# Kernel tuning notes

Measured on AMD Instinct MI355X. Metric: run time of the kernel, lower is better.

Reference implementation:

```python
import jax, jax.numpy as jnp
import numpy as np
from jax import lax

V, E, T, F, K = 100000, 300, 50, 100, 3
B, S = 32, 512


def setup_inputs() -> dict:
    key = jax.random.key(0)
    ks = jax.random.split(key, 10)
    inp = {
        "x": jax.random.randint(ks[0], (B, S), 0, V),
        "tags": jax.random.randint(ks[1], (B, S), 0, T),
        "emb": jax.random.normal(ks[2], (V, E), dtype=jnp.float32),
        "conv_w": jax.random.normal(ks[3], (F, E, K), dtype=jnp.float32) / np.sqrt(E * K),
        "conv_b": jnp.zeros((F,), dtype=jnp.float32),
        "fc_w": jax.random.normal(ks[4], (T, F), dtype=jnp.float32) / np.sqrt(F),
        "fc_b": jnp.zeros((T,), dtype=jnp.float32),
        "start_trans": jax.random.uniform(ks[5], (T,), dtype=jnp.float32, minval=-0.1, maxval=0.1),
        "end_trans": jax.random.uniform(ks[6], (T,), dtype=jnp.float32, minval=-0.1, maxval=0.1),
        "trans": jax.random.uniform(ks[7], (T, T), dtype=jnp.float32, minval=-0.1, maxval=0.1),
    }
    return inp


def _emissions(x, emb, conv_w, conv_b, fc_w, fc_b):
    e = emb[x]                                   # [B,S,E] embedding gather
    e = jnp.transpose(e, (0, 2, 1))              # [B,E,S]
    h = lax.conv_general_dilated(e, conv_w, (1,), [(K // 2, K // 2)])  # [B,F,S] (NCW/OIW)
    h = jax.nn.relu(h + conv_b[None, :, None])   # dropout is identity in eval
    feat = jnp.transpose(h, (0, 2, 1))           # [B,S,F]
    return (jnp.einsum("bsf,tf->bst", feat, fc_w) + fc_b).astype(jnp.float32)  # [B,S,T]


def _crf_nll(emissions, tags, start_trans, end_trans, trans):
    # numerator: score of the gold tag path (full mask)
    em_tag = jnp.take_along_axis(emissions, tags[..., None], axis=-1)[..., 0]  # [B,S]
    num = (start_trans[tags[:, 0]]
           + em_tag.sum(-1)
           + trans[tags[:, :-1], tags[:, 1:]].sum(-1)
           + end_trans[tags[:, -1]])                                           # [B]

    # denominator: forward algorithm via scan over time
    alpha0 = start_trans[None, :] + emissions[:, 0]                             # [B,T]

    def step(alpha, em_t):
        # alpha: [B,T] prev scores; em_t: [B,T] emissions at t
        new = jax.nn.logsumexp(alpha[:, :, None] + trans[None] + em_t[:, None, :], axis=1)
        return new, None

    alpha, _ = lax.scan(step, alpha0, jnp.transpose(emissions[:, 1:], (1, 0, 2)))
    log_z = jax.nn.logsumexp(alpha + end_trans[None, :], axis=-1)               # [B]
    return -(num - log_z).sum()  # torchcrf default reduction='sum'; model returns -llh


def reference(x, tags, emb, conv_w, conv_b, fc_w, fc_b, start_trans, end_trans, trans):
    emissions = _emissions(x, emb, conv_w, conv_b, fc_w, fc_b)
    return _crf_nll(emissions, tags, start_trans, end_trans, trans)
```

## Files before the change

kernel.cpp:

```cpp
#include <hip/hip_runtime.h>
#include <hip/hip_bf16.h>
#include <math.h>

#define BB 32
#define SS 512
#define EE 300
#define FF 100
#define TT 50
#define CH 16
#define NC 32

typedef __attribute__((ext_vector_type(8))) short v8s;
typedef __attribute__((ext_vector_type(4))) float v4f;
#define MFMA16 __builtin_amdgcn_mfma_f32_16x16x32_bf16

#define AP 328
#define NCH 10
#define CKS 3
#define CHB (128 * 96)
#define A2P 136
#define MP 72

__device__ inline unsigned short f2bf(float v) {
    unsigned u = __float_as_uint(v);
    unsigned r = u + 0x7fff + ((u >> 16) & 1);
    return (unsigned short)(r >> 16);
}
__device__ inline float bf2f(short s) {
    return __uint_as_float(((unsigned)(unsigned short)s) << 16);
}
__device__ inline unsigned pkbf2(float a, float b) {
    __hip_bfloat162 h = __float22bfloat162_rn(make_float2(a, b));
    return *(unsigned*)&h;
}
__device__ inline v8s ldsld8(const short* p) {
    return *(const v8s*)__builtin_assume_aligned(p, 16);
}
__device__ inline void g2lds16(const void* g, void* l) {
    __builtin_amdgcn_global_load_lds(
        (const __attribute__((address_space(1))) unsigned int*)g,
        (__attribute__((address_space(3))) unsigned int*)l, 16, 0, 0);
}

__global__ void prep_kernel(const float* __restrict__ tr, const float* __restrict__ cw,
                            const float* __restrict__ fcw,
                            unsigned short* __restrict__ wB2,
                            unsigned short* __restrict__ fcwT2,
                            unsigned short* __restrict__ AT,
                            unsigned short* __restrict__ Ab,
                            float* __restrict__ accum, unsigned* __restrict__ cnt)
{
    const int gid = blockIdx.x * 256 + threadIdx.x;
    const int gs  = 64 * 256;
    if (gid == 0) { *accum = 0.f; *cnt = 0u; }
    for (int idx = gid; idx < NCH * CKS * 8 * 512; idx += gs) {
        int e = idx & 7, p = (idx >> 3) & 63, blk = idx >> 9;
        int ch = blk / 24, rem = blk - ch * 24;
        int sl = rem >> 3, ft = rem & 7;
        int col = p >> 2, q = p & 3;
        int n  = ft * 16 + col;
        int gk = ch * 96 + sl * 32 + q * 8 + e;
        int kk = gk / 320, ee = gk - kk * 320;
        float v = (n < FF && ee < EE) ? cw[n * 900 + ee * 3 + kk] : 0.f;
        wB2[idx] = f2bf(v);
    }
    for (int idx = gid; idx < 16 * 512; idx += gs) {
        int e = idx & 7, p = (idx >> 3) & 63, blk = idx >> 9;
        int ks = blk >> 2, nt = blk & 3;
        int col = p >> 2, q = p & 3;
        int t = nt * 16 + col, f = ks * 32 + q * 8 + e;
        float v = (t < TT && f < FF) ? fcw[t * FF + f] : 0.f;
        fcwT2[idx] = f2bf(v);
    }
    for (int idx = gid; idx < 64 * 64; idx += gs) {
        int r = idx >> 6, c2 = idx & 63;
        AT[idx] = (r < TT && c2 < TT) ? f2bf(__expf(tr[c2 * TT + r])) : 0;
        Ab[idx] = (r < TT && c2 < TT) ? f2bf(__expf(tr[r * TT + c2])) : 0;
    }
}

__global__ __launch_bounds__(256, 3) void emis_kernel(
    const int* __restrict__ x, const float* __restrict__ emb,
    const unsigned short* __restrict__ wB2, const float* __restrict__ cb,
    const unsigned short* __restrict__ fcwT2, const float* __restrict__ fcb,
    const int* __restrict__ tags,
    float* __restrict__ expem, float* __restrict__ rmv, float* __restrict__ emtag)
{
    __shared__ __align__(16) short ldsA[34 * AP];
    __shared__ __align__(16) short ldsB[CHB];

    const int b    = blockIdx.y;
    const int s0   = blockIdx.x * 32;
    const int tid  = threadIdx.x;
    const int wv   = tid >> 6;
    const int lane = tid & 63;
    const int col  = lane & 15;
    const int q    = lane >> 4;
    const int bofs = ((col << 2) | q) << 3;

#pragma unroll
    for (int it = 0; it < 6; ++it) {
        int seg = it * 4 + wv;
        g2lds16((const char*)wB2 + seg * 1024 + lane * 16,
                (char*)ldsB + seg * 1024);
    }

    int   xr[10], ofs[10], e0a[10];
#pragma unroll
    for (int it = 0; it < 10; ++it) {
        int g = tid + it * 256;
        int r = g / 75, eg = g - r * 75;
        int e0 = eg * 4;
        int src = s0 - 1 + r;
        bool v = (g < 2550) && (src >= 0) && (src < SS);
        xr[it]  = v ? x[b * SS + src] : -1;
        ofs[it] = r * AP + e0;
        e0a[it] = e0;
    }
    float4 vv[10];
#pragma unroll
    for (int it = 0; it < 10; ++it)
        vv[it] = (xr[it] >= 0)
               ? *(const float4*)(emb + (size_t)xr[it] * EE + e0a[it])
               : make_float4(0.f, 0.f, 0.f, 0.f);
#pragma unroll
    for (int it = 0; it < 10; ++it) {
        int g = tid + it * 256;
        if (g < 2550) {
            unsigned lo = pkbf2(vv[it].x, vv[it].y);
            unsigned hi = pkbf2(vv[it].z, vv[it].w);
            *(uint2*)&ldsA[ofs[it]] = make_uint2(lo, hi);
        }
    }
    if (tid < 34 * 5) {
        int r = tid / 5, c0 = 300 + (tid % 5) * 4;
        *(short4*)&ldsA[r * AP + c0] = make_short4(0, 0, 0, 0);
    }

    v4f acc[2][2];
#pragma unroll
    for (int a = 0; a < 2; ++a)
#pragma unroll
        for (int f = 0; f < 2; ++f) acc[a][f] = (v4f){0.f, 0.f, 0.f, 0.f};

    const int ftA = wv * 2, ftB = wv * 2 + 1;
    for (int ch = 0; ch < NCH; ++ch) {
        __syncthreads();
#pragma unroll
        for (int sl = 0; sl < CKS; ++sl) {
            int gk = ch * 96 + sl * 32;
            int kk = (gk >= 640) ? 2 : (gk >= 320 ? 1 : 0);
            int e0 = gk - kk * 320;
            v8s a0 = ldsld8(&ldsA[(col + kk) * AP + e0 + q * 8]);
            v8s a1 = ldsld8(&ldsA[(16 + col + kk) * AP + e0 + q * 8]);
            v8s b0 = ldsld8(&ldsB[((sl * 8 + ftA) << 9) + bofs]);
            v8s b1 = ldsld8(&ldsB[((sl * 8 + ftB) << 9) + bofs]);
            acc[0][0] = MFMA16(a0, b0, acc[0][0], 0, 0, 0);
            acc[0][1] = MFMA16(a0, b1, acc[0][1], 0, 0, 0);
            acc[1][0] = MFMA16(a1, b0, acc[1][0], 0, 0, 0);
            acc[1][1] = MFMA16(a1, b1, acc[1][1], 0, 0, 0);
        }
        __syncthreads();
        if (ch < NCH - 1) {
            const char* g = (const char*)(wB2 + (size_t)(ch + 1) * CHB);
#pragma unroll
            for (int it = 0; it < 6; ++it) {
                int seg = it * 4 + wv;
                g2lds16(g + seg * 1024 + lane * 16, (char*)ldsB + seg * 1024);
            }
        }
    }

    short* A2 = ldsA;
    short* B2 = ldsB;
#pragma unroll
    for (int it = 0; it < 4; ++it) {
        int seg = it * 4 + wv;
        g2lds16((const char*)fcwT2 + seg * 1024 + lane * 16,
                (char*)B2 + seg * 1024);
    }
#pragma unroll
    for (int st = 0; st < 2; ++st)
#pragma unroll
        for (int fi = 0; fi < 2; ++fi) {
            int f = (wv * 2 + fi) * 16 + col;
            float bias = (f < FF) ? cb[f] : 0.f;
#pragma unroll
            for (int rg = 0; rg < 4; ++rg) {
                int s = st * 16 + q * 4 + rg;
                float v = (f < FF) ? fmaxf(acc[st][fi][rg] + bias, 0.f) : 0.f;
                A2[s * A2P + f] = (short)f2bf(v);
            }
        }
    __syncthreads();

    if (wv < 2) {
        v4f a2[4];
#pragma unroll
        for (int nt = 0; nt < 4; ++nt) a2[nt] = (v4f){0.f, 0.f, 0.f, 0.f};
#pragma unroll
        for (int ks = 0; ks < 4; ++ks) {
            v8s af = ldsld8(&A2[(wv * 16 + col) * A2P + ks * 32 + q * 8]);
#pragma unroll
            for (int nt = 0; nt < 4; ++nt) {
                v8s bt = ldsld8(&B2[((ks * 4 + nt) << 9) + bofs]);
                a2[nt] = MFMA16(af, bt, a2[nt], 0, 0, 0);
            }
        }
        float fb0 = fcb[col], fb1 = fcb[16 + col], fb2 = fcb[32 + col];
        float fb3 = (col < 2) ? fcb[48 + col] : 0.f;
#pragma unroll
        for (int rg = 0; rg < 4; ++rg) {
            int s = s0 + wv * 16 + q * 4 + rg;
            float e0v = a2[0][rg] + fb0;
            float e1v = a2[1][rg] + fb1;
            float e2v = a2[2][rg] + fb2;
            float e3v = (col < 2) ? a2[3][rg] + fb3 : -1e30f;
            float m = fmaxf(fmaxf(e0v, e1v), fmaxf(e2v, e3v));
#pragma unroll
            for (int off = 1; off < 16; off <<= 1) m = fmaxf(m, __shfl_xor(m, off));
            int gidx = b * SS + s;
            if (col == 0) rmv[gidx] = m;
            int tg = tags[gidx];
            float* orow = expem + (size_t)gidx * TT;
            orow[col]      = __expf(e0v - m);
            orow[16 + col] = __expf(e1v - m);
            orow[32 + col] = __expf(e2v - m);
            if (col < 2) orow[48 + col] = __expf(e3v - m);
            if (tg == col)            emtag[gidx] = e0v;
            else if (tg == 16 + col)  emtag[gidx] = e1v;
            else if (tg == 32 + col)  emtag[gidx] = e2v;
            else if (col < 2 && tg == 48 + col) emtag[gidx] = e3v;
        }
    }
}

__global__ __launch_bounds__(64) void chunk_kernel(
    const float* __restrict__ expem, const unsigned short* __restrict__ AT,
    const unsigned short* __restrict__ Ab,
    unsigned short* __restrict__ R, float* __restrict__ lsR)
{
    __shared__ __align__(16) short L[2][64 * MP];
    __shared__ __align__(16) float emL[CH][64];
    const int c = blockIdx.x, b = blockIdx.y;
    const int lane = threadIdx.x;
    const int col = lane & 15, q = lane >> 4;
    const int t0 = c * CH + 1;
    const int nf = (c == NC - 1) ? (SS - 1 - (NC - 1) * CH) : CH;

    for (int idx = lane; idx < CH * 64; idx += 64) {
        int k = idx >> 6, m = idx & 63;
        float v = 0.f;
        if (m < TT && k < nf) v = expem[((size_t)(b * SS + t0 + k)) * TT + m];
        emL[k][m] = v;
    }

    v8s af[4][2];
#pragma unroll
    for (int jt = 0; jt < 4; ++jt)
#pragma unroll
        for (int kc = 0; kc < 2; ++kc)
            af[jt][kc] = *(const v8s*)(AT + (jt * 16 + col) * 64 + kc * 32 + q * 8);
    __syncthreads();

    {
        const v8s* arow = (const v8s*)(Ab + lane * 64);
#pragma unroll
        for (int g = 0; g < 8; ++g) {
            v8s a = arow[g];
            float f[8];
#pragma unroll
            for (int e = 0; e < 8; ++e) f[e] = bf2f(a[e]) * emL[0][g * 8 + e];
            uint4 o = make_uint4(pkbf2(f[0], f[1]), pkbf2(f[2], f[3]),
                                 pkbf2(f[4], f[5]), pkbf2(f[6], f[7]));
            *(uint4*)&L[0][lane * MP + g * 8] = o;
        }
    }

    int cur = 0;
    for (int k = 1; k < nf; ++k) {
        __syncthreads();
        v8s bf[4][2];
#pragma unroll
        for (int nt = 0; nt < 4; ++nt)
#pragma unroll
            for (int kc = 0; kc < 2; ++kc)
                bf[nt][kc] = ldsld8(&L[cur][(nt * 16 + col) * MP + kc * 32 + q * 8]);
        v4f acc[4][4];
#pragma unroll
        for (int jt = 0; jt < 4; ++jt)
#pragma unroll
            for (int nt = 0; nt < 4; ++nt) {
                acc[jt][nt] = (v4f){0.f, 0.f, 0.f, 0.f};
                acc[jt][nt] = MFMA16(af[jt][0], bf[nt][0], acc[jt][nt], 0, 0, 0);
                acc[jt][nt] = MFMA16(af[jt][1], bf[nt][1], acc[jt][nt], 0, 0, 0);
            }
        if (k < nf - 1) {
#pragma unroll
            for (int jt = 0; jt < 4; ++jt) {
                const float4 em4 = *(const float4*)&emL[k][jt * 16 + q * 4];
#pragma unroll
                for (int nt = 0; nt < 4; ++nt) {
                    uint2 o = make_uint2(
                        pkbf2(acc[jt][nt][0] * em4.x, acc[jt][nt][1] * em4.y),
                        pkbf2(acc[jt][nt][2] * em4.z, acc[jt][nt][3] * em4.w));
                    *(uint2*)&L[cur ^ 1][(nt * 16 + col) * MP + jt * 16 + q * 4] = o;
                }
            }
            cur ^= 1;
        } else {
            float vals[4][4][4];
            float mx = 0.f;
#pragma unroll
            for (int jt = 0; jt < 4; ++jt) {
                const float4 em4 = *(const float4*)&emL[k][jt * 16 + q * 4];
#pragma unroll
                for (int nt = 0; nt < 4; ++nt) {
                    vals[jt][nt][0] = acc[jt][nt][0] * em4.x;
                    vals[jt][nt][1] = acc[jt][nt][1] * em4.y;
                    vals[jt][nt][2] = acc[jt][nt][2] * em4.z;
                    vals[jt][nt][3] = acc[jt][nt][3] * em4.w;
#pragma unroll
                    for (int r = 0; r < 4; ++r) mx = fmaxf(mx, vals[jt][nt][r]);
                }
            }
#pragma unroll
            for (int off = 1; off < 64; off <<= 1) mx = fmaxf(mx, __shfl_xor(mx, off));
            mx = fmaxf(mx, 1e-37f);
            float inv = 1.f / mx;
            unsigned short* Rc = R + ((size_t)(b * NC + c) << 12);
#pragma unroll
            for (int jt = 0; jt < 4; ++jt)
#pragma unroll
                for (int nt = 0; nt < 4; ++nt)
#pragma unroll
                    for (int r = 0; r < 4; ++r)
                        Rc[(jt * 16 + q * 4 + r) * 64 + nt * 16 + col] =
                            f2bf(vals[jt][nt][r] * inv);
            if (lane == 0) lsR[b * NC + c] = __logf(mx);
        }
    }
}

__global__ __launch_bounds__(256) void chain_kernel(
    const float* __restrict__ expem, const unsigned short* __restrict__ R,
    const float* __restrict__ lsR, const float* __restrict__ start,
    const float* __restrict__ endt,
    const float* __restrict__ emtag, const float* __restrict__ rmv,
    const int* __restrict__ tags, const float* __restrict__ tr,
    float* __restrict__ accum, unsigned* __restrict__ cnt,
    float* __restrict__ out)
{
    __shared__ __align__(16) float pvec[64];
    __shared__ float red[8];
    __shared__ float lzsh;
    const int b = blockIdx.x, tid = threadIdx.x;
    const int wv = tid >> 6, i = tid & 63;

    if (wv == 0) {
        pvec[i] = (i < TT) ? __expf(start[i]) * expem[((size_t)(b * SS)) * TT + i] : 0.f;
        const unsigned short* Rb = R + ((size_t)(b * NC) << 12);
        v8s rb[3][8];
#pragma unroll
        for (int pc = 0; pc < 3; ++pc)
#pragma unroll
            for (int g = 0; g < 8; ++g)
                rb[pc][g] = *(const v8s*)(Rb + ((size_t)pc << 12) + i * 64 + g * 8);
        float logacc = 0.f;
#pragma unroll
        for (int c = 0; c < NC; ++c) {
            const int slot = c % 3;
            float acc = 0.f;
            const float4* pv = (const float4*)pvec;
#pragma unroll
            for (int g = 0; g < 8; ++g) {
                v8s v = rb[slot][g];
                float4 pA = pv[g * 2], pB = pv[g * 2 + 1];
                acc = fmaf(bf2f(v[0]), pA.x, acc);
                acc = fmaf(bf2f(v[1]), pA.y, acc);
                acc = fmaf(bf2f(v[2]), pA.z, acc);
                acc = fmaf(bf2f(v[3]), pA.w, acc);
                acc = fmaf(bf2f(v[4]), pB.x, acc);
                acc = fmaf(bf2f(v[5]), pB.y, acc);
                acc = fmaf(bf2f(v[6]), pB.z, acc);
                acc = fmaf(bf2f(v[7]), pB.w, acc);
            }
            if (c + 3 < NC) {
                const unsigned short* Rn = Rb + ((size_t)(c + 3) << 12);
#pragma unroll
                for (int g = 0; g < 8; ++g)
                    rb[slot][g] = *(const v8s*)(Rn + i * 64 + g * 8);
            }
            float mx = acc;
#pragma unroll
            for (int off = 1; off < 64; off <<= 1) mx = fmaxf(mx, __shfl_xor(mx, off));
            mx = fmaxf(mx, 1e-37f);
            logacc += __logf(mx) + lsR[b * NC + c];
            pvec[i] = acc * (1.f / mx);
        }
        float sv = (i < TT) ? pvec[i] * __expf(endt[i]) : 0.f;
#pragma unroll
        for (int off = 1; off < 64; off <<= 1) sv += __shfl_xor(sv, off);
        if (i == 0) lzsh = logacc + __logf(sv);
    } else {
        float accN = 0.f, accR = 0.f;
        for (int s = tid - 64; s < SS; s += 192) {
            int gi = b * SS + s;
            accN += emtag[gi];
            accR += rmv[gi];
            int tg = tags[gi];
            if (s < SS - 1) accN += tr[tg * TT + tags[gi + 1]];
        }
#pragma unroll
        for (int off = 1; off < 64; off <<= 1) {
            accN += __shfl_xor(accN, off);
            accR += __shfl_xor(accR, off);
        }
        if (i == 0) { red[wv] = accN; red[4 + wv] = accR; }
    }
    __syncthreads();
    if (tid == 0) {
        float tn  = red[1] + red[2] + red[3];
        float trm = red[5] + red[6] + red[7];
        float num = tn + start[tags[b * SS]] + endt[tags[b * SS + SS - 1]];
        float nll = trm + lzsh - num;
        atomicAdd(accum, nll);
        __threadfence();
        unsigned old = atomicAdd(cnt, 1u);
        if (old == BB - 1) out[0] = atomicAdd(accum, 0.f);
    }
}

extern "C" void kernel_launch(void* const* d_in, const int* in_sizes, int n_in,
                              void* d_out, int out_size, void* d_ws, size_t ws_size,
                              hipStream_t stream)
{
    const int*   x    = (const int*)d_in[0];
    const int*   tags = (const int*)d_in[1];
    const float* emb  = (const float*)d_in[2];
    const float* cw   = (const float*)d_in[3];
    const float* cb   = (const float*)d_in[4];
    const float* fcw  = (const float*)d_in[5];
    const float* fcb  = (const float*)d_in[6];
    const float* st   = (const float*)d_in[7];
    const float* en   = (const float*)d_in[8];
    const float* tr   = (const float*)d_in[9];

    unsigned short* wB2   = (unsigned short*)d_ws;
    unsigned short* fcwT2 = wB2 + NCH * CKS * 8 * 512;
    unsigned short* ATm   = fcwT2 + 16 * 512;
    unsigned short* Abm   = ATm + 4096;
    unsigned short* Rm    = Abm + 4096;
    float* fbase   = (float*)(Rm + (size_t)BB * NC * 4096);
    float* expem   = fbase;
    float* rmv     = expem + (size_t)BB * SS * TT;
    float* emtag   = rmv + BB * SS;
    float* lsR     = emtag + BB * SS;
    float* accum   = lsR + BB * NC;
    unsigned* cnt  = (unsigned*)(accum + 1);

    prep_kernel<<<dim3(64), 256, 0, stream>>>(tr, cw, fcw, wB2, fcwT2, ATm, Abm,
                                              accum, cnt);
    emis_kernel<<<dim3(16, BB), 256, 0, stream>>>(x, emb, wB2, cb, fcwT2, fcb,
                                                  tags, expem, rmv, emtag);
    chunk_kernel<<<dim3(NC, BB), 64, 0, stream>>>(expem, ATm, Abm, Rm, lsR);
    chain_kernel<<<dim3(BB), 256, 0, stream>>>(expem, Rm, lsR, st, en,
                                               emtag, rmv, tags, tr,
                                               accum, cnt, (float*)d_out);
}
```

Baseline: 241.1 us.

## Fold prep into emissions kernel and chain into chunk kernel via flags

Result: slower. 527.7 us (+118.9%).

```diff
diff --git a/kernel.cpp b/kernel.cpp
--- a/kernel.cpp
+++ b/kernel.cpp
@@ -20,6 +20,7 @@
 #define CHB (128 * 96)
 #define A2P 136
 #define MP 72
+#define MAGICU 0x13572468u
 
 __device__ inline unsigned short f2bf(float v) {
     unsigned u = __float_as_uint(v);
@@ -42,67 +43,68 @@
         (__attribute__((address_space(3))) unsigned int*)l, 16, 0, 0);
 }
 
-__global__ void prep_kernel(const float* __restrict__ tr, const float* __restrict__ cw,
-                            const float* __restrict__ fcw,
-                            unsigned short* __restrict__ wB2,
-                            unsigned short* __restrict__ fcwT2,
-                            unsigned short* __restrict__ AT,
-                            unsigned short* __restrict__ Ab,
-                            float* __restrict__ accum, unsigned* __restrict__ cnt)
-{
-    const int gid = blockIdx.x * 256 + threadIdx.x;
-    const int gs  = 64 * 256;
-    if (gid == 0) { *accum = 0.f; *cnt = 0u; }
-    for (int idx = gid; idx < NCH * CKS * 8 * 512; idx += gs) {
-        int e = idx & 7, p = (idx >> 3) & 63, blk = idx >> 9;
-        int ch = blk / 24, rem = blk - ch * 24;
-        int sl = rem >> 3, ft = rem & 7;
-        int col = p >> 2, q = p & 3;
-        int n  = ft * 16 + col;
-        int gk = ch * 96 + sl * 32 + q * 8 + e;
-        int kk = gk / 320, ee = gk - kk * 320;
-        float v = (n < FF && ee < EE) ? cw[n * 900 + ee * 3 + kk] : 0.f;
-        wB2[idx] = f2bf(v);
-    }
-    for (int idx = gid; idx < 16 * 512; idx += gs) {
-        int e = idx & 7, p = (idx >> 3) & 63, blk = idx >> 9;
-        int ks = blk >> 2, nt = blk & 3;
-        int col = p >> 2, q = p & 3;
-        int t = nt * 16 + col, f = ks * 32 + q * 8 + e;
-        float v = (t < TT && f < FF) ? fcw[t * FF + f] : 0.f;
-        fcwT2[idx] = f2bf(v);
-    }
-    for (int idx = gid; idx < 64 * 64; idx += gs) {
-        int r = idx >> 6, c2 = idx & 63;
-        AT[idx] = (r < TT && c2 < TT) ? f2bf(__expf(tr[c2 * TT + r])) : 0;
-        Ab[idx] = (r < TT && c2 < TT) ? f2bf(__expf(tr[r * TT + c2])) : 0;
-    }
-}
-
 __global__ __launch_bounds__(256, 3) void emis_kernel(
     const int* __restrict__ x, const float* __restrict__ emb,
-    const unsigned short* __restrict__ wB2, const float* __restrict__ cb,
-    const unsigned short* __restrict__ fcwT2, const float* __restrict__ fcb,
-    const int* __restrict__ tags,
+    const float* __restrict__ cw, const float* __restrict__ cb,
+    const float* __restrict__ fcw, const float* __restrict__ fcb,
+    const float* __restrict__ tr, const int* __restrict__ tags,
+    unsigned short* __restrict__ wB2, unsigned short* __restrict__ fcwT2,
+    unsigned short* __restrict__ AT, unsigned short* __restrict__ Ab,
+    unsigned* __restrict__ flags, unsigned* __restrict__ done,
+    float* __restrict__ accum, unsigned* __restrict__ cnt,
     float* __restrict__ expem, float* __restrict__ rmv, float* __restrict__ emtag)
 {
     __shared__ __align__(16) short ldsA[34 * AP];
     __shared__ __align__(16) short ldsB[CHB];
 
-    const int b    = blockIdx.y;
-    const int s0   = blockIdx.x * 32;
-    const int tid  = threadIdx.x;
-    const int wv   = tid >> 6;
-    const int lane = tid & 63;
-    const int col  = lane & 15;
-    const int q    = lane >> 4;
-    const int bofs = ((col << 2) | q) << 3;
-
-#pragma unroll
-    for (int it = 0; it < 6; ++it) {
-        int seg = it * 4 + wv;
-        g2lds16((const char*)wB2 + seg * 1024 + lane * 16,
-                (char*)ldsB + seg * 1024);
+    const int b      = blockIdx.y;
+    const int s0     = blockIdx.x * 32;
+    const int tid    = threadIdx.x;
+    const int wv     = tid >> 6;
+    const int lane   = tid & 63;
+    const int col    = lane & 15;
+    const int q      = lane >> 4;
+    const int bofs   = ((col << 2) | q) << 3;
+    const int linear = blockIdx.y * 16 + blockIdx.x;
+
+    if (linear < 64) {
+        const int gid = linear * 256 + tid;
+        const int gs  = 64 * 256;
+        for (int idx = gid; idx < NCH * CKS * 8 * 512; idx += gs) {
+            int e = idx & 7, p = (idx >> 3) & 63, blk = idx >> 9;
+            int ch = blk / 24, rem = blk - ch * 24;
+            int sl = rem >> 3, ft = rem & 7;
+            int pc = p >> 2, pq = p & 3;
+            int n  = ft * 16 + pc;
+            int gk = ch * 96 + sl * 32 + pq * 8 + e;
+            int kk = gk / 320, ee = gk - kk * 320;
+            float v = (n < FF && ee < EE) ? cw[n * 900 + ee * 3 + kk] : 0.f;
+            wB2[idx] = f2bf(v);
+        }
+        for (int idx = gid; idx < 16 * 512; idx += gs) {
+            int e = idx & 7, p = (idx >> 3) & 63, blk = idx >> 9;
+            int ks = blk >> 2, nt = blk & 3;
+            int pc = p >> 2, pq = p & 3;
+            int t = nt * 16 + pc, f = ks * 32 + pq * 8 + e;
+            float v = (t < TT && f < FF) ? fcw[t * FF + f] : 0.f;
+            fcwT2[idx] = f2bf(v);
+        }
+        for (int idx = gid; idx < 64 * 64; idx += gs) {
+            int r = idx >> 6, c2 = idx & 63;
+            AT[idx] = (r < TT && c2 < TT) ? f2bf(__expf(tr[c2 * TT + r])) : 0;
+            Ab[idx] = (r < TT && c2 < TT) ? f2bf(__expf(tr[r * TT + c2])) : 0;
+        }
+        __syncthreads();
+        if (tid == 0) {
+            __threadfence();
+            __hip_atomic_store(&flags[linear], MAGICU,
+                               __ATOMIC_RELEASE, __HIP_MEMORY_SCOPE_AGENT);
+        }
+    }
+    if (linear == 0) {
+        if (tid < BB) done[tid] = 0u;
+        else if (tid == BB) *accum = 0.f;
+        else if (tid == BB + 1) *cnt = 0u;
     }
 
     int   xr[10], ofs[10], e0a[10];
@@ -135,6 +137,19 @@
     if (tid < 34 * 5) {
         int r = tid / 5, c0 = 300 + (tid % 5) * 4;
         *(short4*)&ldsA[r * AP + c0] = make_short4(0, 0, 0, 0);
+    }
+
+    if (tid == 0) {
+        for (int i = 0; i < 64; ++i)
+            while (__hip_atomic_load(&flags[i], __ATOMIC_ACQUIRE,
+                                     __HIP_MEMORY_SCOPE_AGENT) != MAGICU) {}
+    }
+    __syncthreads();
+#pragma unroll
+    for (int it = 0; it < 6; ++it) {
+        int seg = it * 4 + wv;
+        g2lds16((const char*)wB2 + seg * 1024 + lane * 16,
+                (char*)ldsB + seg * 1024);
     }
 
     v4f acc[2][2];
@@ -238,7 +253,13 @@
 __global__ __launch_bounds__(64) void chunk_kernel(
     const float* __restrict__ expem, const unsigned short* __restrict__ AT,
     const unsigned short* __restrict__ Ab,
-    unsigned short* __restrict__ R, float* __restrict__ lsR)
+    const float* __restrict__ emtag, const float* __restrict__ rmv,
+    const int* __restrict__ tags, const float* __restrict__ tr,
+    const float* __restrict__ start, const float* __restrict__ endt,
+    unsigned short* __restrict__ R, float* __restrict__ lsR,
+    float* __restrict__ part, unsigned* __restrict__ done,
+    float* __restrict__ accum, unsigned* __restrict__ cnt,
+    float* __restrict__ out)
 {
     __shared__ __align__(16) short L[2][64 * MP];
     __shared__ __align__(16) float emL[CH][64];
@@ -248,6 +269,19 @@
     const int t0 = c * CH + 1;
     const int nf = (c == NC - 1) ? (SS - 1 - (NC - 1) * CH) : CH;
 
+    {
+        int s = c * CH + lane;
+        float pc = 0.f;
+        if (lane < CH) {
+            int gi = b * SS + s;
+            pc = rmv[gi] - emtag[gi];
+            if (s < SS - 1) pc -= tr[tags[gi] * TT + tags[gi + 1]];
+        }
+#pragma unroll
+        for (int off = 1; off < 16; off <<= 1) pc += __shfl_xor(pc, off);
+        if (lane == 0) part[b * NC + c] = pc;
+    }
+
     for (int idx = lane; idx < CH * 64; idx += 64) {
         int k = idx >> 6, m = idx & 63;
         float v = 0.f;
@@ -340,94 +374,72 @@
             if (lane == 0) lsR[b * NC + c] = __logf(mx);
         }
     }
-}
-
-__global__ __launch_bounds__(256) void chain_kernel(
-    const float* __restrict__ expem, const unsigned short* __restrict__ R,
-    const float* __restrict__ lsR, const float* __restrict__ start,
-    const float* __restrict__ endt,
-    const float* __restrict__ emtag, const float* __restrict__ rmv,
-    const int* __restrict__ tags, const float* __restrict__ tr,
-    float* __restrict__ accum, unsigned* __restrict__ cnt,
-    float* __restrict__ out)
-{
-    __shared__ __align__(16) float pvec[64];
-    __shared__ float red[8];
-    __shared__ float lzsh;
-    const int b = blockIdx.x, tid = threadIdx.x;
-    const int wv = tid >> 6, i = tid & 63;
-
-    if (wv == 0) {
-        pvec[i] = (i < TT) ? __expf(start[i]) * expem[((size_t)(b * SS)) * TT + i] : 0.f;
-        const unsigned short* Rb = R + ((size_t)(b * NC) << 12);
-        v8s rb[3][8];
-#pragma unroll
-        for (int pc = 0; pc < 3; ++pc)
+
+    int old = 0;
+    if (lane == 0) {
+        __threadfence();
+        old = (int)atomicAdd(&done[b], 1u);
+    }
+    old = __shfl(old, 0);
+    if (old != NC - 1) return;
+    __threadfence();
+
+    float* pvec = (float*)emL;
+    pvec[lane] = (lane < TT) ? __expf(start[lane]) * expem[((size_t)(b * SS)) * TT + lane] : 0.f;
+    const unsigned short* Rb = R + ((size_t)(b * NC) << 12);
+    v8s rb[3][8];
+#pragma unroll
+    for (int pc = 0; pc < 3; ++pc)
+#pragma unroll
+        for (int g = 0; g < 8; ++g)
+            rb[pc][g] = *(const v8s*)(Rb + ((size_t)pc << 12) + lane * 64 + g * 8);
+    float logacc = 0.f;
+#pragma unroll
+    for (int cc = 0; cc < NC; ++cc) {
+        const int slot = cc % 3;
+        float acc = 0.f;
+        const float4* pv = (const float4*)pvec;
+#pragma unroll
+        for (int g = 0; g < 8; ++g) {
+            v8s v = rb[slot][g];
+            float4 pA = pv[g * 2], pB = pv[g * 2 + 1];
+            acc = fmaf(bf2f(v[0]), pA.x, acc);
+            acc = fmaf(bf2f(v[1]), pA.y, acc);
+            acc = fmaf(bf2f(v[2]), pA.z, acc);
+            acc = fmaf(bf2f(v[3]), pA.w, acc);
+            acc = fmaf(bf2f(v[4]), pB.x, acc);
+            acc = fmaf(bf2f(v[5]), pB.y, acc);
+            acc = fmaf(bf2f(v[6]), pB.z, acc);
+            acc = fmaf(bf2f(v[7]), pB.w, acc);
+        }
+        if (cc + 3 < NC) {
+            const unsigned short* Rn = Rb + ((size_t)(cc + 3) << 12);
 #pragma unroll
             for (int g = 0; g < 8; ++g)
-                rb[pc][g] = *(const v8s*)(Rb + ((size_t)pc << 12) + i * 64 + g * 8);
-        float logacc = 0.f;
-#pragma unroll
-        for (int c = 0; c < NC; ++c) {
-            const int slot = c % 3;
-            float acc = 0.f;
-            const float4* pv = (const float4*)pvec;
-#pragma unroll
-            for (int g = 0; g < 8; ++g) {
-                v8s v = rb[slot][g];
-                float4 pA = pv[g * 2], pB = pv[g * 2 + 1];
-                acc = fmaf(bf2f(v[0]), pA.x, acc);
-                acc = fmaf(bf2f(v[1]), pA.y, acc);
-                acc = fmaf(bf2f(v[2]), pA.z, acc);
-                acc = fmaf(bf2f(v[3]), pA.w, acc);
-                acc = fmaf(bf2f(v[4]), pB.x, acc);
-                acc = fmaf(bf2f(v[5]), pB.y, acc);
-                acc = fmaf(bf2f(v[6]), pB.z, acc);
-                acc = fmaf(bf2f(v[7]), pB.w, acc);
-            }
-            if (c + 3 < NC) {
-                const unsigned short* Rn = Rb + ((size_t)(c + 3) << 12);
-#pragma unroll
-                for (int g = 0; g < 8; ++g)
-                    rb[slot][g] = *(const v8s*)(Rn + i * 64 + g * 8);
-            }
-            float mx = acc;
-#pragma unroll
-            for (int off = 1; off < 64; off <<= 1) mx = fmaxf(mx, __shfl_xor(mx, off));
-            mx = fmaxf(mx, 1e-37f);
-            logacc += __logf(mx) + lsR[b * NC + c];
-            pvec[i] = acc * (1.f / mx);
-        }
-        float sv = (i < TT) ? pvec[i] * __expf(endt[i]) : 0.f;
-#pragma unroll
-        for (int off = 1; off < 64; off <<= 1) sv += __shfl_xor(sv, off);
-        if (i == 0) lzsh = logacc + __logf(sv);
-    } else {
-        float accN = 0.f, accR = 0.f;
-        for (int s = tid - 64; s < SS; s += 192) {
-            int gi = b * SS + s;
-            accN += emtag[gi];
-            accR += rmv[gi];
-            int tg = tags[gi];
-            if (s < SS - 1) accN += tr[tg * TT + tags[gi + 1]];
-        }
-#pragma unroll
-        for (int off = 1; off < 64; off <<= 1) {
-            accN += __shfl_xor(accN, off);
-            accR += __shfl_xor(accR, off);
-        }
-        if (i == 0) { red[wv] = accN; red[4 + wv] = accR; }
-    }
-    __syncthreads();
-    if (tid == 0) {
-        float tn  = red[1] + red[2] + red[3];
-        float trm = red[5] + red[6] + red[7];
-        float num = tn + start[tags[b * SS]] + endt[tags[b * SS + SS - 1]];
-        float nll = trm + lzsh - num;
+                rb[slot][g] = *(const v8s*)(Rn + lane * 64 + g * 8);
+        }
+        float mx = acc;
+#pragma unroll
+        for (int off = 1; off < 64; off <<= 1) mx = fmaxf(mx, __shfl_xor(mx, off));
+        mx = fmaxf(mx, 1e-37f);
+        logacc += __logf(mx) + lsR[b * NC + cc];
+        pvec[lane] = acc * (1.f / mx);
+    }
+    float sv = (lane < TT) ? pvec[lane] * __expf(endt[lane]) : 0.f;
+#pragma unroll
+    for (int off = 1; off < 64; off <<= 1) sv += __shfl_xor(sv, off);
+    float lz = logacc + __logf(sv);
+
+    float np = (lane < NC) ? part[b * NC + lane] : 0.f;
+#pragma unroll
+    for (int off = 1; off < 32; off <<= 1) np += __shfl_xor(np, off);
+
+    if (lane == 0) {
+        float nll = lz + np - start[tags[b * SS]] - endt[tags[b * SS + SS - 1]];
         atomicAdd(accum, nll);
         __threadfence();
-        unsigned old = atomicAdd(cnt, 1u);
-        if (old == BB - 1) out[0] = atomicAdd(accum, 0.f);
+        unsigned o2 = atomicAdd(cnt, 1u);
+        if (o2 == BB - 1) out[0] = atomicAdd(accum, 0.f);
     }
 }
 
@@ -456,15 +468,17 @@
     float* rmv     = expem + (size_t)BB * SS * TT;
     float* emtag   = rmv + BB * SS;
     float* lsR     = emtag + BB * SS;
-    float* accum   = lsR + BB * NC;
+    float* part    = lsR + BB * NC;
+    float* accum   = part + BB * NC;
     unsigned* cnt  = (unsigned*)(accum + 1);
-
-    prep_kernel<<<dim3(64), 256, 0, stream>>>(tr, cw, fcw, wB2, fcwT2, ATm, Abm,
-                                              accum, cnt);
-    emis_kernel<<<dim3(16, BB), 256, 0, stream>>>(x, emb, wB2, cb, fcwT2, fcb,
-                                                  tags, expem, rmv, emtag);
-    chunk_kernel<<<dim3(NC, BB), 64, 0, stream>>>(expem, ATm, Abm, Rm, lsR);
-    chain_kernel<<<dim3(BB), 256, 0, stream>>>(expem, Rm, lsR, st, en,
-                                               emtag, rmv, tags, tr,
-                                               accum, cnt, (float*)d_out);
-}
+    unsigned* done = cnt + 1;
+    unsigned* flags = done + BB;
+
+    emis_kernel<<<dim3(16, BB), 256, 0, stream>>>(
+        x, emb, cw, cb, fcw, fcb, tr, tags,
+        wB2, fcwT2, ATm, Abm, flags, done, accum, cnt,
+        expem, rmv, emtag);
+    chunk_kernel<<<dim3(NC, BB), 64, 0, stream>>>(
+        expem, ATm, Abm, emtag, rmv, tags, tr, st, en,
+        Rm, lsR, part, done, accum, cnt, (float*)d_out);
+}
```
